# Kernel tuning notes

Hardware: AMD Instinct MI355X
Metric: run time of the kernel (lower is better)

The kernel has to match this reference:

```python
import jax, jax.numpy as jnp
import numpy as np

B, T, DIM, H, E, D, K = 2, 2048, 1024, 8, 5, 64, 3


def setup_inputs() -> dict:
    key = jax.random.key(0)
    ks = jax.random.split(key, 7)
    s = 0.02
    return {
        "x": jax.random.normal(ks[0], (B, T, DIM), dtype=jnp.float32),
        "w_q": jax.random.normal(ks[1], (DIM, H * E * D), dtype=jnp.float32) * s,
        "w_kv": jax.random.normal(ks[2], (DIM, 2 * H * E * D), dtype=jnp.float32) * s,
        "w_s": jax.random.normal(ks[3], (DIM, H * E), dtype=jnp.float32) * s,
        "w_d": jax.random.normal(ks[4], (DIM, H * E), dtype=jnp.float32) * s,
        "w_o_w": jax.random.normal(ks[5], (H, DIM, D), dtype=jnp.float32) * s,
        "w_o_b": jax.random.normal(ks[6], (H, DIM), dtype=jnp.float32) * s,
    }


def _select(proj_full, eps, s):
    # Faithful to torch scatter_(3, eps, s): value s[..., k] is written at
    # expert slot eps[..., k]; multiplying the full projection by that sparse
    # score tensor and summing over e == gather selected experts, weight by
    # the FIRST K raw scores (not the topk values), and sum.
    sel = jnp.take_along_axis(proj_full, eps[..., None], axis=3)  # b t h K d
    return (sel * s[..., :K, None]).sum(axis=3)  # b t h d


def reference(x, w_q, w_kv, w_s, w_d, w_o_w, w_o_b):
    scale = D ** (-0.5)
    ss = jax.nn.sigmoid(x @ w_s).reshape(B, T, H, E)
    sd = jax.nn.sigmoid(x @ w_d).reshape(B, T, H, E)
    eps_s = jax.lax.top_k(ss, K)[1]  # b t h K
    eps_d = jax.lax.top_k(sd, K)[1]

    q_full = (x @ w_q).reshape(B, T, H, E, D)
    q = _select(q_full, eps_d, sd)  # b t h d

    kv_full = (x @ w_kv).reshape(B, T, 2, H, E, D)
    k = _select(kv_full[:, :, 0], eps_s, ss)
    v = _select(kv_full[:, :, 1], eps_s, ss)

    attn = jnp.einsum("bihd,bjhd->bhij", q * scale, k)
    probs = jax.nn.softmax(attn, axis=-1)
    out = jnp.einsum("bhij,bjhd->bihd", probs, v)  # b t h d

    # per-head Linear(dim_head, dim) then sum over heads (stack+sum)
    return jnp.einsum("bihd,hfd->bif", out, w_o_w) + w_o_b.sum(axis=0)
```

## Files before the change

kernel.cpp:

```cpp
#include <hip/hip_runtime.h>

#define DEV __device__ __forceinline__

typedef float f32x4 __attribute__((ext_vector_type(4)));
typedef short s16x8 __attribute__((ext_vector_type(8)));
typedef unsigned short u16;
typedef unsigned int u32;

constexpr int Bb = 2, Tt = 2048, DIMc = 1024, Hh = 8, Ee = 5, Dd = 64;
constexpr int NTOK = Bb * Tt;
constexpr int NQ = Hh * Ee * Dd;

DEV u16 f2bf(float f) {
  union { float f; u32 u; } v; v.f = f;
  u32 r = v.u + 0x7fffu + ((v.u >> 16) & 1u);
  return (u16)(r >> 16);
}

DEV u32 pk2(float a, float b) {
  return (u32)f2bf(a) | ((u32)f2bf(b) << 16);
}

DEV s16x8 ld8(const u16* p) {
  uint4 u = *reinterpret_cast<const uint4*>(p);
  return __builtin_bit_cast(s16x8, u);
}

DEV f32x4 mfma16(s16x8 a, s16x8 b, f32x4 c) {
  return __builtin_amdgcn_mfma_f32_16x16x32_bf16(a, b, c, 0, 0, 0);
}

DEV void gld16(const void* g, void* l) {
  __builtin_amdgcn_global_load_lds(
      (const __attribute__((address_space(1))) void*)g,
      (__attribute__((address_space(3))) void*)l, 16, 0, 0);
}

__launch_bounds__(256)
__global__ void k_prep(const float* __restrict__ x, const float* __restrict__ wq,
                       const float* __restrict__ wkv, const float* __restrict__ wow,
                       const float* __restrict__ wob, const float* __restrict__ wsr,
                       const float* __restrict__ wdr,
                       u16* __restrict__ xb, u16* __restrict__ wT,
                       u16* __restrict__ woT, float* __restrict__ bsum,
                       float* __restrict__ wsdT) {
  int bid = blockIdx.x, t = threadIdx.x;
  if (bid < 4096) {
    int i = bid * 256 + t;
    float4 v = reinterpret_cast<const float4*>(x)[i];
    u16 r0 = f2bf(v.x), r1 = f2bf(v.y), r2 = f2bf(v.z), r3 = f2bf(v.w);
    u32 lo = (u32)r0 | ((u32)r1 << 16);
    u32 hi = (u32)r2 | ((u32)r3 << 16);
    reinterpret_cast<uint2*>(xb)[i] = make_uint2(lo, hi);
  } else if (bid < 11776) {
    int b2 = bid - 4096;
    int R0 = (b2 % 240) * 32;
    int C0 = (b2 / 240) * 32;
    int s = R0 / 2560, rem = R0 % 2560;
    int h = rem / 320, n0 = rem % 320;
    const float* src; int ld; int col0;
    if (s == 0) { src = wq;  ld = 2560; col0 = h * 320 + n0; }
    else        { src = wkv; ld = 5120; col0 = (s - 1) * 2560 + h * 320 + n0; }
    __shared__ float tile[32][33];
    int tx = t & 31, ty = t >> 5;
    #pragma unroll
    for (int i = 0; i < 4; i++) {
      int c = C0 + ty + 8 * i;
      tile[ty + 8 * i][tx] = src[(size_t)c * ld + col0 + tx];
    }
    __syncthreads();
    #pragma unroll
    for (int i = 0; i < 4; i++) {
      int n = ty + 8 * i;
      wT[(size_t)(R0 + n) * 1024 + C0 + tx] = f2bf(tile[tx][n]);
    }
  } else if (bid < 12032) {
    int b2 = bid - 11776;
    int f = b2 * 4 + (t >> 6), d = t & 63;
    #pragma unroll
    for (int h = 0; h < 8; h++)
      woT[(size_t)f * 512 + h * 64 + d] = f2bf(wow[((size_t)h * 1024 + f) * 64 + d]);
  } else if (bid < 12036) {
    int f = (bid - 12032) * 256 + t;
    float s = 0.f;
    #pragma unroll
    for (int h = 0; h < 8; h++) s += wob[h * 1024 + f];
    bsum[f] = s;
  } else {
    int j = bid - 12036;
    const float* src = (j < 40) ? wsr : wdr;
    int c = (j < 40) ? j : j - 40;
    for (int i = t; i < 1024; i += 256)
      wsdT[(size_t)j * 1024 + i] = src[(size_t)i * 40 + c];
  }
}

__launch_bounds__(320)
__global__ void k_scores(const float* __restrict__ x, const float* __restrict__ wsdT,
                         int* __restrict__ eps_s, int* __restrict__ eps_d,
                         float* __restrict__ ss3, float* __restrict__ sd3) {
  int tokb = blockIdx.x * 8;
  __shared__ float xl[8][1028];
  __shared__ float sc[8][80];
  const float4* xsrc = reinterpret_cast<const float4*>(x + (size_t)tokb * 1024);
  for (int i = threadIdx.x; i < 2048; i += 320) {
    int tok = i >> 8, col4 = i & 255;
    *reinterpret_cast<float4*>(&xl[tok][col4 * 4]) = xsrc[i];
  }
  __syncthreads();
  {
    int tok = threadIdx.x & 7, j = threadIdx.x >> 3;
    const float4* wsp = reinterpret_cast<const float4*>(wsdT + (size_t)j * 1024);
    const float4* wdp = reinterpret_cast<const float4*>(wsdT + (size_t)(j + 40) * 1024);
    float as0 = 0.f, as1 = 0.f, ad0 = 0.f, ad1 = 0.f;
    #pragma unroll 4
    for (int k4 = 0; k4 < 256; k4 += 2) {
      float4 x0 = *reinterpret_cast<const float4*>(&xl[tok][k4 * 4]);
      float4 x1 = *reinterpret_cast<const float4*>(&xl[tok][k4 * 4 + 4]);
      float4 wsv0 = wsp[k4], wsv1 = wsp[k4 + 1];
      float4 wdv0 = wdp[k4], wdv1 = wdp[k4 + 1];
      as0 += x0.x * wsv0.x + x0.y * wsv0.y + x0.z * wsv0.z + x0.w * wsv0.w;
      as1 += x1.x * wsv1.x + x1.y * wsv1.y + x1.z * wsv1.z + x1.w * wsv1.w;
      ad0 += x0.x * wdv0.x + x0.y * wdv0.y + x0.z * wdv0.z + x0.w * wdv0.w;
      ad1 += x1.x * wdv1.x + x1.y * wdv1.y + x1.z * wdv1.z + x1.w * wdv1.w;
    }
    float as = as0 + as1, ad = ad0 + ad1;
    sc[tok][j]      = 1.f / (1.f + expf(-as));
    sc[tok][40 + j] = 1.f / (1.f + expf(-ad));
  }
  __syncthreads();
  int t2 = threadIdx.x;
  if (t2 < 128) {
    int tt = t2 >> 4, u = t2 & 15, h = u >> 1, which = u & 1;
    const float* S = &sc[tt][which * 40 + h * 5];
    float v[5];
    #pragma unroll
    for (int e = 0; e < 5; e++) v[e] = S[e];
    int tok = tokb + tt;
    int base = (tok * 8 + h) * 3;
    int* eps = which ? eps_d : eps_s;
    float* w3 = which ? sd3 : ss3;
    bool used[5] = {false, false, false, false, false};
    #pragma unroll
    for (int kk = 0; kk < 3; kk++) {
      float best = -1e30f; int bi = 0;
      #pragma unroll
      for (int e = 0; e < 5; e++)
        if (!used[e] && v[e] > best) { best = v[e]; bi = e; }
      used[bi] = true;
      eps[base + kk] = bi;
    }
    #pragma unroll
    for (int kk = 0; kk < 3; kk++) w3[base + kk] = S[kk];
  }
}

__launch_bounds__(512)
__global__ void k_proj(const u16* __restrict__ xb, const u16* __restrict__ wT,
                       const int* __restrict__ eps_d, const int* __restrict__ eps_s,
                       const float* __restrict__ sd3, const float* __restrict__ ss3,
                       u16* __restrict__ qw, u16* __restrict__ kw, u16* __restrict__ vw) {
  int tok0 = blockIdx.x * 128;
  int h = blockIdx.y;
  int s = blockIdx.z;
  int Rbase = (s * 8 + h) * 320;
  __shared__ alignas(16) u16 bsA[128 * 64];
  __shared__ alignas(16) u16 bsB[320 * 64];
  int wv = threadIdx.x >> 6, l = threadIdx.x & 63;
  int g = l >> 4, c = l & 15;
  f32x4 acc[20];
  #pragma unroll
  for (int i = 0; i < 20; i++) acc[i] = (f32x4){0.f, 0.f, 0.f, 0.f};

  const u16* wTp0 = wT + (size_t)Rbase * 1024;
  const u16* xbp0 = xb + (size_t)tok0 * 1024;

  for (int k0 = 0; k0 < 1024; k0 += 64) {
    __syncthreads();
    const u16* wTp = wTp0 + k0;
    #pragma unroll
    for (int j = 0; j < 5; j++) {
      int ch = wv * 320 + j * 64 + l;
      int row = ch >> 3, part = ch & 7;
      gld16(wTp + (size_t)row * 1024 + ((part * 8) ^ ((row & 7) * 8)),
            &bsB[(wv * 320 + j * 64) * 8]);
    }
    const u16* xbp = xbp0 + k0;
    #pragma unroll
    for (int j = 0; j < 2; j++) {
      int ch = wv * 128 + j * 64 + l;
      int row = ch >> 3, part = ch & 7;
      gld16(xbp + (size_t)row * 1024 + ((part * 8) ^ ((row & 7) * 8)),
            &bsA[(wv * 128 + j * 64) * 8]);
    }
    __syncthreads();

    #pragma unroll
    for (int kk = 0; kk < 2; kk++) {
      int off = (kk * 32 + g * 8) ^ ((c & 7) * 8);
      s16x8 a = *reinterpret_cast<const s16x8*>(&bsA[(wv * 16 + c) * 64 + off]);
      #pragma unroll
      for (int nt = 0; nt < 20; nt++) {
        s16x8 b = *reinterpret_cast<const s16x8*>(&bsB[(nt * 16 + c) * 64 + off]);
        acc[nt] = mfma16(a, b, acc[nt]);
      }
    }
  }

  const int* eps = (s == 0) ? eps_d : eps_s;
  const float* w3 = (s == 0) ? sd3 : ss3;
  float scale = (s == 0) ? 0.125f : 1.0f;
  u16* dst = (s == 0) ? qw : (s == 1 ? kw : vw);
  #pragma unroll
  for (int r = 0; r < 4; r++) {
    int tokr = tok0 + wv * 16 + g * 4 + r;
    int base = (tokr * 8 + h) * 3;
    int e0 = eps[base], e1 = eps[base + 1], e2 = eps[base + 2];
    float w0 = w3[base], w1 = w3[base + 1], w2 = w3[base + 2];
    float we[5];
    #pragma unroll
    for (int e = 0; e < 5; e++)
      we[e] = (e0 == e ? w0 : 0.f) + (e1 == e ? w1 : 0.f) + (e2 == e ? w2 : 0.f);
    int b = tokr >> 11, t = tokr & 2047;
    size_t obase = (((size_t)b * 8 + h) * 2048 + t) * 64;
    #pragma unroll
    for (int dh = 0; dh < 4; dh++) {
      float vq = 0.f;
      #pragma unroll
      for (int e = 0; e < 5; e++) vq += we[e] * acc[e * 4 + dh][r];
      dst[obase + dh * 16 + c] = f2bf(vq * scale);
    }
  }
}

__global__ void k_trv(const u16* __restrict__ vw, u16* __restrict__ vT) {
  int bh = blockIdx.z;
  int t0 = blockIdx.x * 32, d0 = blockIdx.y * 32;
  __shared__ u16 tile[32][33];
  const u16* src = vw + (size_t)bh * 2048 * 64;
  u16* dst = vT + (size_t)bh * 64 * 2048;
  int tx = threadIdx.x, ty = threadIdx.y;
  #pragma unroll
  for (int i = 0; i < 4; i++)
    tile[ty + 8 * i][tx] = src[(size_t)(t0 + ty + 8 * i) * 64 + d0 + tx];
  __syncthreads();
  int p = 8 * ((tx & 15) >> 2) + (tx & 3) + ((tx >= 16) ? 4 : 0);
  #pragma unroll
  for (int i = 0; i < 4; i++)
    dst[(size_t)(d0 + ty + 8 * i) * 2048 + t0 + p] = tile[tx][ty + 8 * i];
}

__launch_bounds__(256)
__global__ void k_attn(const u16* __restrict__ qw, const u16* __restrict__ kw,
                       const u16* __restrict__ vT, u16* __restrict__ ow) {
  int bh = blockIdx.y;
  int b = bh >> 3, h = bh & 7;
  int q0 = blockIdx.x * 64;
  int wv = threadIdx.x >> 6, l = threadIdx.x & 63;
  int g = l >> 4, c = l & 15;
  const u16* qp = qw + (size_t)bh * 2048 * 64;
  const u16* kp = kw + (size_t)bh * 2048 * 64;
  const u16* vp = vT + (size_t)bh * 64 * 2048;
  __shared__ alignas(16) u16 Kl[128 * 64];
  __shared__ alignas(16) u16 Vl[64 * 128];

  s16x8 qa0 = ld8(qp + (size_t)(q0 + wv * 16 + c) * 64 + 0 + 8 * g);
  s16x8 qa1 = ld8(qp + (size_t)(q0 + wv * 16 + c) * 64 + 32 + 8 * g);

  f32x4 o[4];
  #pragma unroll
  for (int i = 0; i < 4; i++) o[i] = (f32x4){0.f, 0.f, 0.f, 0.f};
  float ssum = 0.f;

  for (int kt = 0; kt < 2048; kt += 128) {
    __syncthreads();
    #pragma unroll
    for (int j = 0; j < 4; j++) {
      int ch = (wv * 4 + j) * 64 + l;
      int row = ch >> 3, sl = ch & 7;
      gld16(kp + (size_t)(kt + row) * 64 + ((sl ^ (row & 7)) * 8),
            &Kl[(wv * 4 + j) * 64 * 8]);
    }
    #pragma unroll
    for (int j = 0; j < 4; j++) {
      int ch = (wv * 4 + j) * 64 + l;
      int d = ch >> 4, sl = ch & 15;
      gld16(vp + (size_t)d * 2048 + kt + ((sl ^ (d & 15)) * 8),
            &Vl[(wv * 4 + j) * 64 * 8]);
    }
    __syncthreads();

    #pragma unroll
    for (int kk = 0; kk < 4; kk++) {
      int r0 = kk * 32 + c, r1 = kk * 32 + 16 + c;
      int c7 = c & 7;
      s16x8 ka0 = *reinterpret_cast<const s16x8*>(&Kl[r0 * 64 + ((0 + g) ^ c7) * 8]);
      s16x8 ka1 = *reinterpret_cast<const s16x8*>(&Kl[r0 * 64 + ((4 + g) ^ c7) * 8]);
      s16x8 kc0 = *reinterpret_cast<const s16x8*>(&Kl[r1 * 64 + ((0 + g) ^ c7) * 8]);
      s16x8 kc1 = *reinterpret_cast<const s16x8*>(&Kl[r1 * 64 + ((4 + g) ^ c7) * 8]);

      f32x4 s0 = (f32x4){0.f, 0.f, 0.f, 0.f};
      f32x4 s1 = (f32x4){0.f, 0.f, 0.f, 0.f};
      s0 = mfma16(ka0, qa0, s0);
      s0 = mfma16(ka1, qa1, s0);
      s1 = mfma16(kc0, qa0, s1);
      s1 = mfma16(kc1, qa1, s1);

      float p00 = __expf(s0[0]), p01 = __expf(s0[1]);
      float p02 = __expf(s0[2]), p03 = __expf(s0[3]);
      float p10 = __expf(s1[0]), p11 = __expf(s1[1]);
      float p12 = __expf(s1[2]), p13 = __expf(s1[3]);
      ssum += (p00 + p01) + (p02 + p03) + (p10 + p11) + (p12 + p13);

      uint4 pw = make_uint4(pk2(p00, p01), pk2(p02, p03),
                            pk2(p10, p11), pk2(p12, p13));
      s16x8 pa = __builtin_bit_cast(s16x8, pw);

      #pragma unroll
      for (int nt = 0; nt < 4; nt++) {
        int d = nt * 16 + c;
        s16x8 vb = *reinterpret_cast<const s16x8*>(&Vl[d * 128 + (((kk * 4 + g) ^ (d & 15)) * 8)]);
        o[nt] = mfma16(pa, vb, o[nt]);
      }
    }
  }

  ssum += __shfl_xor(ssum, 16, 64);
  ssum += __shfl_xor(ssum, 32, 64);
  #pragma unroll
  for (int r = 0; r < 4; r++) {
    float sm = __shfl(ssum, g * 4 + r, 64);
    float inv = 1.f / sm;
    int t = q0 + wv * 16 + g * 4 + r;
    #pragma unroll
    for (int nt = 0; nt < 4; nt++)
      ow[((size_t)(b * 2048 + t)) * 512 + h * 64 + nt * 16 + c] = f2bf(o[nt][r] * inv);
  }
}

__launch_bounds__(512)
__global__ void k_oproj(const u16* __restrict__ ow, const u16* __restrict__ woT,
                        const float* __restrict__ biasum, float* __restrict__ out) {
  int t0 = blockIdx.x * 128, f0 = blockIdx.y * 64;
  int wv = threadIdx.x >> 6, l = threadIdx.x & 63;
  int g = l >> 4, c = l & 15;
  f32x4 acc[4];
  #pragma unroll
  for (int i = 0; i < 4; i++) acc[i] = (f32x4){0.f, 0.f, 0.f, 0.f};
  for (int k0 = 0; k0 < 512; k0 += 32) {
    s16x8 a = ld8(ow + (size_t)(t0 + wv * 16 + c) * 512 + k0 + 8 * g);
    #pragma unroll
    for (int nt = 0; nt < 4; nt++) {
      s16x8 bfr = ld8(woT + (size_t)(f0 + nt * 16 + c) * 512 + k0 + 8 * g);
      acc[nt] = mfma16(a, bfr, acc[nt]);
    }
  }
  #pragma unroll
  for (int r = 0; r < 4; r++) {
    int t = t0 + wv * 16 + g * 4 + r;
    #pragma unroll
    for (int nt = 0; nt < 4; nt++) {
      int f = f0 + nt * 16 + c;
      out[(size_t)t * 1024 + f] = acc[nt][r] + biasum[f];
    }
  }
}

extern "C" void kernel_launch(void* const* d_in, const int* in_sizes, int n_in,
                              void* d_out, int out_size, void* d_ws, size_t ws_size,
                              hipStream_t stream) {
  const float* x    = (const float*)d_in[0];
  const float* w_q  = (const float*)d_in[1];
  const float* w_kv = (const float*)d_in[2];
  const float* w_s  = (const float*)d_in[3];
  const float* w_d  = (const float*)d_in[4];
  const float* w_ow = (const float*)d_in[5];
  const float* w_ob = (const float*)d_in[6];
  float* out = (float*)d_out;

  char* ws = (char*)d_ws;
  size_t o = 0;
  u16* xb     = (u16*)(ws + o); o += (size_t)NTOK * DIMc * 2;
  u16* wT     = (u16*)(ws + o); o += (size_t)3 * NQ * DIMc * 2;
  u16* woT    = (u16*)(ws + o); o += (size_t)1024 * 512 * 2;
  float* bsum = (float*)(ws + o); o += 4096;
  float* wsdT = (float*)(ws + o); o += (size_t)80 * 1024 * 4;
  int* eps_s  = (int*)(ws + o); o += (size_t)NTOK * 8 * 3 * 4;
  int* eps_d  = (int*)(ws + o); o += (size_t)NTOK * 8 * 3 * 4;
  float* ss3  = (float*)(ws + o); o += (size_t)NTOK * 8 * 3 * 4;
  float* sd3  = (float*)(ws + o); o += (size_t)NTOK * 8 * 3 * 4;
  u16* qw     = (u16*)(ws + o); o += (size_t)NTOK * 512 * 2;
  u16* kw     = (u16*)(ws + o); o += (size_t)NTOK * 512 * 2;
  u16* vw     = (u16*)(ws + o); o += (size_t)NTOK * 512 * 2;
  u16* vTw    = (u16*)(ws + o); o += (size_t)NTOK * 512 * 2;
  u16* oww    = (u16*)(ws + o); o += (size_t)NTOK * 512 * 2;

  k_prep<<<12116, 256, 0, stream>>>(x, w_q, w_kv, w_ow, w_ob, w_s, w_d,
                                    xb, wT, woT, bsum, wsdT);
  k_scores<<<512, 320, 0, stream>>>(x, wsdT, eps_s, eps_d, ss3, sd3);
  k_proj<<<dim3(32, 8, 3), 512, 0, stream>>>(xb, wT, eps_d, eps_s, sd3, ss3, qw, kw, vw);
  k_trv<<<dim3(64, 2, 16), dim3(32, 8), 0, stream>>>(vw, vTw);
  k_attn<<<dim3(32, 16), 256, 0, stream>>>(qw, kw, vTw, oww);
  k_oproj<<<dim3(32, 16), 512, 0, stream>>>(oww, woT, bsum, out);
}
```

Baseline: 217.7 us.

## Split attention key range across two wave groups per block

Doubles the attention block to 512 threads: two groups of four waves each process half of the key sequence for the same 64 queries, using separate K/V shared buffers. Partial outputs and softmax sums are combined through shared memory at the end before normalisation. This raises the number of waves in flight and halves the serial key loop length per wave, at the cost of double LDS use and an extra reduction step.

```diff
diff --git a/kernel.cpp b/kernel.cpp
--- a/kernel.cpp
+++ b/kernel.cpp
@@ -250,43 +250,46 @@
     dst[(size_t)(d0 + ty + 8 * i) * 2048 + t0 + p] = tile[tx][ty + 8 * i];
 }
 
-__launch_bounds__(256)
+__launch_bounds__(512)
 __global__ void k_attn(const u16* __restrict__ qw, const u16* __restrict__ kw,
                        const u16* __restrict__ vT, u16* __restrict__ ow) {
   int bh = blockIdx.y;
   int b = bh >> 3, h = bh & 7;
   int q0 = blockIdx.x * 64;
   int wv = threadIdx.x >> 6, l = threadIdx.x & 63;
+  int seg = wv >> 2, wq = wv & 3;
   int g = l >> 4, c = l & 15;
   const u16* qp = qw + (size_t)bh * 2048 * 64;
   const u16* kp = kw + (size_t)bh * 2048 * 64;
   const u16* vp = vT + (size_t)bh * 64 * 2048;
-  __shared__ alignas(16) u16 Kl[128 * 64];
-  __shared__ alignas(16) u16 Vl[64 * 128];
-
-  s16x8 qa0 = ld8(qp + (size_t)(q0 + wv * 16 + c) * 64 + 0 + 8 * g);
-  s16x8 qa1 = ld8(qp + (size_t)(q0 + wv * 16 + c) * 64 + 32 + 8 * g);
+  __shared__ alignas(16) u16 Kl[2][128 * 64];
+  __shared__ alignas(16) u16 Vl[2][64 * 128];
+
+  s16x8 qa0 = ld8(qp + (size_t)(q0 + wq * 16 + c) * 64 + 0 + 8 * g);
+  s16x8 qa1 = ld8(qp + (size_t)(q0 + wq * 16 + c) * 64 + 32 + 8 * g);
 
   f32x4 o[4];
   #pragma unroll
   for (int i = 0; i < 4; i++) o[i] = (f32x4){0.f, 0.f, 0.f, 0.f};
   float ssum = 0.f;
 
-  for (int kt = 0; kt < 2048; kt += 128) {
+  const int kb0 = seg * 1024;
+  for (int kt = 0; kt < 1024; kt += 128) {
+    int kbase = kb0 + kt;
     __syncthreads();
     #pragma unroll
     for (int j = 0; j < 4; j++) {
-      int ch = (wv * 4 + j) * 64 + l;
+      int ch = (wq * 4 + j) * 64 + l;
       int row = ch >> 3, sl = ch & 7;
-      gld16(kp + (size_t)(kt + row) * 64 + ((sl ^ (row & 7)) * 8),
-            &Kl[(wv * 4 + j) * 64 * 8]);
+      gld16(kp + (size_t)(kbase + row) * 64 + ((sl ^ (row & 7)) * 8),
+            &Kl[seg][(wq * 4 + j) * 64 * 8]);
     }
     #pragma unroll
     for (int j = 0; j < 4; j++) {
-      int ch = (wv * 4 + j) * 64 + l;
+      int ch = (wq * 4 + j) * 64 + l;
       int d = ch >> 4, sl = ch & 15;
-      gld16(vp + (size_t)d * 2048 + kt + ((sl ^ (d & 15)) * 8),
-            &Vl[(wv * 4 + j) * 64 * 8]);
+      gld16(vp + (size_t)d * 2048 + kbase + ((sl ^ (d & 15)) * 8),
+            &Vl[seg][(wq * 4 + j) * 64 * 8]);
     }
     __syncthreads();
 
@@ -294,10 +297,10 @@
     for (int kk = 0; kk < 4; kk++) {
       int r0 = kk * 32 + c, r1 = kk * 32 + 16 + c;
       int c7 = c & 7;
-      s16x8 ka0 = *reinterpret_cast<const s16x8*>(&Kl[r0 * 64 + ((0 + g) ^ c7) * 8]);
-      s16x8 ka1 = *reinterpret_cast<const s16x8*>(&Kl[r0 * 64 + ((4 + g) ^ c7) * 8]);
-      s16x8 kc0 = *reinterpret_cast<const s16x8*>(&Kl[r1 * 64 + ((0 + g) ^ c7) * 8]);
-      s16x8 kc1 = *reinterpret_cast<const s16x8*>(&Kl[r1 * 64 + ((4 + g) ^ c7) * 8]);
+      s16x8 ka0 = *reinterpret_cast<const s16x8*>(&Kl[seg][r0 * 64 + ((0 + g) ^ c7) * 8]);
+      s16x8 ka1 = *reinterpret_cast<const s16x8*>(&Kl[seg][r0 * 64 + ((4 + g) ^ c7) * 8]);
+      s16x8 kc0 = *reinterpret_cast<const s16x8*>(&Kl[seg][r1 * 64 + ((0 + g) ^ c7) * 8]);
+      s16x8 kc1 = *reinterpret_cast<const s16x8*>(&Kl[seg][r1 * 64 + ((4 + g) ^ c7) * 8]);
 
       f32x4 s0 = (f32x4){0.f, 0.f, 0.f, 0.f};
       f32x4 s1 = (f32x4){0.f, 0.f, 0.f, 0.f};
@@ -319,7 +322,7 @@
       #pragma unroll
       for (int nt = 0; nt < 4; nt++) {
         int d = nt * 16 + c;
-        s16x8 vb = *reinterpret_cast<const s16x8*>(&Vl[d * 128 + (((kk * 4 + g) ^ (d & 15)) * 8)]);
+        s16x8 vb = *reinterpret_cast<const s16x8*>(&Vl[seg][d * 128 + (((kk * 4 + g) ^ (d & 15)) * 8)]);
         o[nt] = mfma16(pa, vb, o[nt]);
       }
     }
@@ -327,14 +330,32 @@
 
   ssum += __shfl_xor(ssum, 16, 64);
   ssum += __shfl_xor(ssum, 32, 64);
-  #pragma unroll
-  for (int r = 0; r < 4; r++) {
-    float sm = __shfl(ssum, g * 4 + r, 64);
-    float inv = 1.f / sm;
-    int t = q0 + wv * 16 + g * 4 + r;
-    #pragma unroll
-    for (int nt = 0; nt < 4; nt++)
-      ow[((size_t)(b * 2048 + t)) * 512 + h * 64 + nt * 16 + c] = f2bf(o[nt][r] * inv);
+
+  float* osp  = reinterpret_cast<float*>(&Kl[0][0]);
+  float* sslp = reinterpret_cast<float*>(&Vl[0][0]);
+  __syncthreads();
+  if (g == 0) sslp[seg * 64 + wq * 16 + c] = ssum;
+  if (seg == 1) {
+    #pragma unroll
+    for (int r = 0; r < 4; r++)
+      #pragma unroll
+      for (int nt = 0; nt < 4; nt++)
+        osp[(wq * 16 + g * 4 + r) * 64 + nt * 16 + c] = o[nt][r];
+  }
+  __syncthreads();
+  if (seg == 0) {
+    #pragma unroll
+    for (int r = 0; r < 4; r++) {
+      int q = g * 4 + r;
+      float sm = sslp[wq * 16 + q] + sslp[64 + wq * 16 + q];
+      float inv = 1.f / sm;
+      int t = q0 + wq * 16 + q;
+      #pragma unroll
+      for (int nt = 0; nt < 4; nt++) {
+        float val = (o[nt][r] + osp[(wq * 16 + q) * 64 + nt * 16 + c]) * inv;
+        ow[((size_t)(b * 2048 + t)) * 512 + h * 64 + nt * 16 + c] = f2bf(val);
+      }
+    }
   }
 }
 
@@ -400,6 +421,6 @@
   k_scores<<<512, 320, 0, stream>>>(x, wsdT, eps_s, eps_d, ss3, sd3);
   k_proj<<<dim3(32, 8, 3), 512, 0, stream>>>(xb, wT, eps_d, eps_s, sd3, ss3, qw, kw, vw);
   k_trv<<<dim3(64, 2, 16), dim3(32, 8), 0, stream>>>(vw, vTw);
-  k_attn<<<dim3(32, 16), 256, 0, stream>>>(qw, kw, vTw, oww);
+  k_attn<<<dim3(32, 16), 512, 0, stream>>>(qw, kw, vTw, oww);
   k_oproj<<<dim3(32, 16), 512, 0, stream>>>(oww, woT, bsum, out);
 }
```

New measurement: 211.0 us, median of 2. 3.1% less time.
